# Optimization experiments

Measured on AMD Instinct MI355X. Metric: run time of the kernel, lower is better.

## Reference

```python
import jax, jax.numpy as jnp
import numpy as np

IN_DIMS = 512
TOKEN_DIM = 512
NUM_HEADS = 1
D = TOKEN_DIM * NUM_HEADS
SCALE = TOKEN_DIM ** (-0.5)
EPS = 1e-12  # torch F.normalize default


def _l2norm(v, axis):
    n = jnp.sqrt(jnp.sum(v * v, axis=axis, keepdims=True))
    return v / jnp.maximum(n, EPS)


def setup_inputs() -> dict:
    key = jax.random.key(0)
    ks = jax.random.split(key, 10)
    B, C, H, W = 64, IN_DIMS, 28, 28
    s_in = IN_DIMS ** -0.5
    s_d = D ** -0.5
    return {
        "x": jax.random.normal(ks[0], (B, C, H, W), jnp.float32),
        "Wq": jax.random.normal(ks[1], (IN_DIMS, D), jnp.float32) * s_in,
        "bq": jax.random.normal(ks[2], (D,), jnp.float32) * 0.01,
        "Wk": jax.random.normal(ks[3], (IN_DIMS, D), jnp.float32) * s_in,
        "bk": jax.random.normal(ks[4], (D,), jnp.float32) * 0.01,
        "w_g": jax.random.normal(ks[5], (D, 1), jnp.float32),
        "Wp": jax.random.normal(ks[6], (D, D), jnp.float32) * s_d,
        "bp": jax.random.normal(ks[7], (D,), jnp.float32) * 0.01,
        "Wf": jax.random.normal(ks[8], (D, TOKEN_DIM), jnp.float32) * s_d,
        "bf": jax.random.normal(ks[9], (TOKEN_DIM,), jnp.float32) * 0.01,
    }


def reference(x, Wq, bq, Wk, bk, w_g, Wp, bp, Wf, bf):
    B, C, H, W = x.shape
    t = x.reshape(B, C, H * W).transpose(0, 2, 1)          # [B, N, C]
    query = _l2norm(t @ Wq + bq, axis=-1)                  # [B, N, D]
    k = _l2norm(t @ Wk + bk, axis=-1)                      # [B, N, D]
    attn = _l2norm((query @ w_g) * SCALE, axis=1)          # [B, N, 1], normalized over tokens
    ctx = jnp.sum(attn * query, axis=1, keepdims=True)     # [B, 1, D] global context
    out = (ctx * k) @ Wp + bp + query                      # [B, N, D]
    out = out @ Wf + bf                                    # [B, N, TOKEN_DIM]
    return out.transpose(0, 2, 1).reshape(B, -1, H, W)
```

## Files before the change

kernel.cpp:

```cpp
#include <hip/hip_runtime.h>

#define EPSN 1e-12f
#define SCALE_F 0.044194173824159216f
#define MTOT 50176

typedef __bf16 bf16x8 __attribute__((ext_vector_type(8)));
typedef float  f32x4  __attribute__((ext_vector_type(4)));

__device__ __forceinline__ void gld16(const void* src, void* dst) {
  __builtin_amdgcn_global_load_lds(
      (const __attribute__((address_space(1))) unsigned int*)src,
      (__attribute__((address_space(3))) unsigned int*)dst, 16, 0, 0);
}

__global__ __launch_bounds__(256) void k_xt(const float* __restrict__ x,
                                            __bf16* __restrict__ xT, int b0) {
  __shared__ float T[32][33];
  const int n0 = blockIdx.x * 32, c0 = blockIdx.y * 32;
  const int bl = blockIdx.z, b = b0 + bl;
  const int dx = threadIdx.x, ty = threadIdx.y;
  #pragma unroll
  for (int pp = 0; pp < 4; ++pp) {
    int c = ty + pp * 8;
    int n = n0 + dx;
    T[c][dx] = (n < 784) ? x[((size_t)b * 512 + c0 + c) * 784 + n] : 0.f;
  }
  __syncthreads();
  #pragma unroll
  for (int pp = 0; pp < 4; ++pp) {
    int n = ty + pp * 8;
    if (n0 + n < 784)
      xT[((size_t)bl * 784 + n0 + n) * 512 + c0 + dx] = (__bf16)T[dx][n];
  }
}

__global__ __launch_bounds__(256) void k_prep_t(const float* __restrict__ Wq,
                                                const float* __restrict__ Wk,
                                                __bf16* __restrict__ WqT,
                                                __bf16* __restrict__ WkT) {
  __shared__ float Tq[32][33], Tk[32][33];
  const int c0 = blockIdx.x * 32, d0 = blockIdx.y * 32;
  const int dx = threadIdx.x, cy = threadIdx.y;
  #pragma unroll
  for (int p = 0; p < 4; ++p) {
    int c = cy + p * 8;
    Tq[c][dx] = Wq[(size_t)(c0 + c) * 512 + d0 + dx];
    Tk[c][dx] = Wk[(size_t)(c0 + c) * 512 + d0 + dx];
  }
  __syncthreads();
  #pragma unroll
  for (int p = 0; p < 4; ++p) {
    int d = cy + p * 8;
    WqT[(size_t)(d0 + d) * 512 + c0 + dx] = (__bf16)Tq[dx][d];
    WkT[(size_t)(d0 + d) * 512 + c0 + dx] = (__bf16)Tk[dx][d];
  }
}

__global__ __launch_bounds__(512) void k_prep_w(const float* __restrict__ Wp,
                                                const float* __restrict__ Wf,
                                                const float* __restrict__ bp,
                                                const float* __restrict__ bfv,
                                                __bf16* __restrict__ WcT,
                                                float* __restrict__ bpf) {
  const int kk0 = blockIdx.x * 8;
  const int d = threadIdx.x;
  float acc[8] = {};
  float bacc = 0.f;
  const bool dobp = (blockIdx.x == 0);
  for (int c = 0; c < 512; ++c) {
    float wf = Wf[(size_t)c * 512 + d];
    #pragma unroll
    for (int i = 0; i < 8; ++i) acc[i] = fmaf(Wp[(size_t)(kk0 + i) * 512 + c], wf, acc[i]);
    if (dobp) bacc = fmaf(bp[c], wf, bacc);
  }
  #pragma unroll
  for (int i = 0; i < 8; ++i) {
    WcT[(size_t)d * 1024 + kk0 + i]       = (__bf16)acc[i];
    WcT[(size_t)d * 1024 + 512 + kk0 + i] = (__bf16)Wf[(size_t)(kk0 + i) * 512 + d];
  }
  if (dobp) bpf[d] = bacc + bfv[d];
}

__global__ __launch_bounds__(256, 2) void k_gemm(const __bf16* __restrict__ xT,
                                                 const __bf16* __restrict__ WqT,
                                                 const __bf16* __restrict__ WkT,
                                                 const float* __restrict__ bq,
                                                 const float* __restrict__ bk,
                                                 const float* __restrict__ wg,
                                                 const int b0,
                                                 __bf16* __restrict__ qraw,
                                                 __bf16* __restrict__ kraw,
                                                 float* __restrict__ psqQ,
                                                 float* __restrict__ psqK,
                                                 float* __restrict__ gdo) {
  __shared__ __align__(1024) unsigned char As[8192], BQs[8192], BKs[8192];
  const int t = threadIdx.x, l = t & 63, w = t >> 6;
  const int li = l & 15, lq = l >> 4;
  const int p = blockIdx.x;
  const int xq = p & 7, q2 = p >> 3;
  const int nt = q2 & 3;
  const int g = (q2 >> 2) * 8 + xq;
  const int bl = g / 7, mt = g % 7;
  const int b = b0 + bl;
  const int m0 = mt * 128;

  const int r0 = 2 * w, r1 = r0 + 1;
  int row0 = m0 + r0 * 16 + li; if (row0 > 783) row0 = 783;
  int row1 = m0 + r1 * 16 + li; if (row1 > 783) row1 = 783;
  const __bf16* a0s = xT + ((size_t)bl * 784 + row0) * 512 + lq * 8;
  const __bf16* a1s = xT + ((size_t)bl * 784 + row1) * 512 + lq * 8;
  const __bf16* q0s = WqT + (size_t)(nt * 128 + r0 * 16 + li) * 512 + lq * 8;
  const __bf16* q1s = WqT + (size_t)(nt * 128 + r1 * 16 + li) * 512 + lq * 8;
  const __bf16* k0s = WkT + (size_t)(nt * 128 + r0 * 16 + li) * 512 + lq * 8;
  const __bf16* k1s = WkT + (size_t)(nt * 128 + r1 * 16 + li) * 512 + lq * 8;

  f32x4 accQ[4][4] = {}, accK[4][4] = {};

  for (int ks = 0; ks < 16; ++ks) {
    const int k0 = ks * 32;
    gld16(a0s + k0, As + r0 * 1024);
    gld16(a1s + k0, As + r1 * 1024);
    gld16(q0s + k0, BQs + r0 * 1024);
    gld16(q1s + k0, BQs + r1 * 1024);
    gld16(k0s + k0, BKs + r0 * 1024);
    gld16(k1s + k0, BKs + r1 * 1024);
    __syncthreads();
    bf16x8 af[4];
    #pragma unroll
    for (int rb = 0; rb < 4; ++rb)
      af[rb] = *(const bf16x8*)(As + ((w & 1) * 4 + rb) * 1024 + l * 16);
    #pragma unroll
    for (int cb = 0; cb < 4; ++cb) {
      bf16x8 bq8 = *(const bf16x8*)(BQs + ((w >> 1) * 4 + cb) * 1024 + l * 16);
      #pragma unroll
      for (int rb = 0; rb < 4; ++rb)
        accQ[rb][cb] = __builtin_amdgcn_mfma_f32_16x16x32_bf16(af[rb], bq8, accQ[rb][cb], 0, 0, 0);
      bf16x8 bk8 = *(const bf16x8*)(BKs + ((w >> 1) * 4 + cb) * 1024 + l * 16);
      #pragma unroll
      for (int rb = 0; rb < 4; ++rb)
        accK[rb][cb] = __builtin_amdgcn_mfma_f32_16x16x32_bf16(af[rb], bk8, accK[rb][cb], 0, 0, 0);
    }
    __syncthreads();
  }

  const int colb = nt * 128 + (w >> 1) * 64;
  const int cg = nt * 2 + (w >> 1);
  float bqv[4], bkv[4], wv[4];
  #pragma unroll
  for (int cb = 0; cb < 4; ++cb) {
    int col = colb + cb * 16 + li;
    bqv[cb] = bq[col]; bkv[cb] = bk[col]; wv[cb] = wg[col];
  }
  #pragma unroll
  for (int rb = 0; rb < 4; ++rb)
    #pragma unroll
    for (int j = 0; j < 4; ++j) {
      int rowg = m0 + (w & 1) * 64 + rb * 16 + lq * 4 + j;
      bool ok = rowg < 784;
      size_t token = (size_t)b * 784 + rowg;
      float ssq = 0.f, ssk = 0.f, sg = 0.f;
      #pragma unroll
      for (int cb = 0; cb < 4; ++cb) {
        float vq = accQ[rb][cb][j] + bqv[cb];
        float vk = accK[rb][cb][j] + bkv[cb];
        ssq = fmaf(vq, vq, ssq);
        ssk = fmaf(vk, vk, ssk);
        sg  = fmaf(vq, wv[cb], sg);
        if (ok) {
          qraw[token * 512 + colb + cb * 16 + li] = (__bf16)vq;
          kraw[token * 512 + colb + cb * 16 + li] = (__bf16)vk;
        }
      }
      ssq += __shfl_xor(ssq, 1); ssq += __shfl_xor(ssq, 2); ssq += __shfl_xor(ssq, 4); ssq += __shfl_xor(ssq, 8);
      ssk += __shfl_xor(ssk, 1); ssk += __shfl_xor(ssk, 2); ssk += __shfl_xor(ssk, 4); ssk += __shfl_xor(ssk, 8);
      sg  += __shfl_xor(sg, 1);  sg  += __shfl_xor(sg, 2);  sg  += __shfl_xor(sg, 4);  sg  += __shfl_xor(sg, 8);
      if (ok && li == 0) {
        psqQ[(size_t)cg * MTOT + token] = ssq;
        psqK[(size_t)cg * MTOT + token] = ssk;
        gdo [(size_t)cg * MTOT + token] = sg;
      }
    }
}

__global__ __launch_bounds__(256) void k_normc(const float* __restrict__ psqQ,
                                               const float* __restrict__ psqK,
                                               const float* __restrict__ gdo,
                                               float* __restrict__ invqA,
                                               float* __restrict__ invkA,
                                               float* __restrict__ coefA,
                                               float* __restrict__ gA) {
  const int tkn = blockIdx.x * 256 + threadIdx.x;
  if (tkn >= MTOT) return;
  float sq = 0.f, sk = 0.f, gd = 0.f;
  #pragma unroll
  for (int cg = 0; cg < 8; ++cg) {
    sq += psqQ[(size_t)cg * MTOT + tkn];
    sk += psqK[(size_t)cg * MTOT + tkn];
    gd += gdo[(size_t)cg * MTOT + tkn];
  }
  float invq = 1.f / fmaxf(sqrtf(sq), EPSN);
  float invk = 1.f / fmaxf(sqrtf(sk), EPSN);
  float gv = gd * invq;
  invqA[tkn] = invq;
  invkA[tkn] = invk;
  coefA[tkn] = gv * invq;
  gA[tkn]    = gv;
}

__global__ __launch_bounds__(512) void k_pctx(const __bf16* __restrict__ qraw,
                                              const float* __restrict__ coefA,
                                              const float* __restrict__ gA,
                                              float* __restrict__ ctx) {
  __shared__ float wred[8];
  __shared__ float part[4][128];
  const int ch = blockIdx.x, b = blockIdx.y, t = threadIdx.x;
  const size_t base = (size_t)b * 784;
  float gsq;
  { float gv = gA[base + t]; gsq = gv * gv; }
  if (t + 512 < 784) { float gv = gA[base + t + 512]; gsq = fmaf(gv, gv, gsq); }
  gsq += __shfl_xor(gsq, 1);  gsq += __shfl_xor(gsq, 2);  gsq += __shfl_xor(gsq, 4);
  gsq += __shfl_xor(gsq, 8);  gsq += __shfl_xor(gsq, 16); gsq += __shfl_xor(gsq, 32);
  if ((t & 63) == 0) wred[t >> 6] = gsq;
  __syncthreads();
  float tot = 0.f;
  #pragma unroll
  for (int i = 0; i < 8; ++i) tot += wred[i];
  const float alpha = SCALE_F / fmaxf(sqrtf(tot) * SCALE_F, EPSN);
  const int dof = t & 127, s = t >> 7;
  const int nb = s * 196;
  const __bf16* qb = qraw + (base + nb) * 512 + ch * 128 + dof;
  const float* cf = coefA + base + nb;
  float a0 = 0.f, a1 = 0.f, a2 = 0.f, a3 = 0.f;
  for (int n = 0; n < 196; n += 4) {
    a0 = fmaf(cf[n],     (float)qb[(size_t)n * 512],       a0);
    a1 = fmaf(cf[n + 1], (float)qb[(size_t)(n + 1) * 512], a1);
    a2 = fmaf(cf[n + 2], (float)qb[(size_t)(n + 2) * 512], a2);
    a3 = fmaf(cf[n + 3], (float)qb[(size_t)(n + 3) * 512], a3);
  }
  part[s][dof] = (a0 + a1) + (a2 + a3);
  __syncthreads();
  if (t < 128) {
    float sum = part[0][t] + part[1][t] + part[2][t] + part[3][t];
    ctx[(size_t)b * 512 + ch * 128 + t] = alpha * sum;
  }
}

__global__ __launch_bounds__(256, 3) void k_out(const __bf16* __restrict__ qraw,
                                                const __bf16* __restrict__ kraw,
                                                const float* __restrict__ invqA,
                                                const float* __restrict__ invkA,
                                                const float* __restrict__ ctx,
                                                const __bf16* __restrict__ WcT,
                                                const float* __restrict__ bpf,
                                                float* __restrict__ out) {
  __shared__ __align__(1024) unsigned char As[8192], Bs[8192];
  __shared__ float ctx_l[512];
  const int t = threadIdx.x, l = t & 63, w = t >> 6;
  const int li = l & 15, lq = l >> 4;
  const int p = blockIdx.x;
  const int xq = p & 7, q2 = p >> 3;
  const int nt = q2 & 3;
  const int g = (q2 >> 2) * 8 + xq;
  const int b = g / 7, mt = g % 7;
  const int m0 = mt * 128;

  ctx_l[t]       = ctx[(size_t)b * 512 + t];
  ctx_l[t + 256] = ctx[(size_t)b * 512 + t + 256];

  const int rA0 = w, rA1 = w + 4;
  int row0 = m0 + rA0 * 16 + li; if (row0 > 783) row0 = 783;
  int row1 = m0 + rA1 * 16 + li; if (row1 > 783) row1 = 783;
  const size_t tk0 = (size_t)b * 784 + row0, tk1 = (size_t)b * 784 + row1;
  const float iq0 = invqA[tk0], ik0 = invkA[tk0];
  const float iq1 = invqA[tk1], ik1 = invkA[tk1];
  const __bf16* wpB0 = WcT + (size_t)(nt * 128 + (2 * w) * 16 + li) * 1024 + lq * 8;
  const __bf16* wpB1 = WcT + (size_t)(nt * 128 + (2 * w + 1) * 16 + li) * 1024 + lq * 8;

  f32x4 acc[4][4] = {};
  __syncthreads();

  for (int ks = 0; ks < 32; ++ks) {
    const int k0 = ks * 32;
    gld16(wpB0 + k0, Bs + (2 * w) * 1024);
    gld16(wpB1 + k0, Bs + (2 * w + 1) * 1024);
    {
      const bool dk = ks < 16;
      const __bf16* ap = dk ? kraw : qraw;
      const int kk = (k0 & 511) + lq * 8;
      bf16x8 v0 = *(const bf16x8*)(ap + tk0 * 512 + kk);
      bf16x8 v1 = *(const bf16x8*)(ap + tk1 * 512 + kk);
      const float s0 = dk ? ik0 : iq0, s1 = dk ? ik1 : iq1;
      bf16x8 o0, o1;
      if (dk) {
        f32x4 c0 = *(const f32x4*)&ctx_l[kk];
        f32x4 c1 = *(const f32x4*)&ctx_l[kk + 4];
        #pragma unroll
        for (int j = 0; j < 4; ++j) {
          o0[j]     = (__bf16)((float)v0[j]     * s0 * c0[j]);
          o0[4 + j] = (__bf16)((float)v0[4 + j] * s0 * c1[j]);
          o1[j]     = (__bf16)((float)v1[j]     * s1 * c0[j]);
          o1[4 + j] = (__bf16)((float)v1[4 + j] * s1 * c1[j]);
        }
      } else {
        #pragma unroll
        for (int j = 0; j < 8; ++j) {
          o0[j] = (__bf16)((float)v0[j] * s0);
          o1[j] = (__bf16)((float)v1[j] * s1);
        }
      }
      *(bf16x8*)(As + rA0 * 1024 + l * 16) = o0;
      *(bf16x8*)(As + rA1 * 1024 + l * 16) = o1;
    }
    __syncthreads();
    bf16x8 af[4];
    #pragma unroll
    for (int rb = 0; rb < 4; ++rb)
      af[rb] = *(const bf16x8*)(As + ((w & 1) * 4 + rb) * 1024 + l * 16);
    #pragma unroll
    for (int cb = 0; cb < 4; ++cb) {
      bf16x8 bf = *(const bf16x8*)(Bs + ((w >> 1) * 4 + cb) * 1024 + l * 16);
      #pragma unroll
      for (int rb = 0; rb < 4; ++rb)
        acc[rb][cb] = __builtin_amdgcn_mfma_f32_16x16x32_bf16(af[rb], bf, acc[rb][cb], 0, 0, 0);
    }
    __syncthreads();
  }

  const int colb = nt * 128 + (w >> 1) * 64;
  float bv[4];
  #pragma unroll
  for (int cb = 0; cb < 4; ++cb) bv[cb] = bpf[colb + cb * 16 + li];
  #pragma unroll
  for (int rb = 0; rb < 4; ++rb) {
    int nrow = m0 + (w & 1) * 64 + rb * 16 + lq * 4;
    if (nrow < 784) {
      #pragma unroll
      for (int cb = 0; cb < 4; ++cb) {
        f32x4 v;
        #pragma unroll
        for (int j = 0; j < 4; ++j) v[j] = acc[rb][cb][j] + bv[cb];
        *(f32x4*)&out[((size_t)b * 512 + colb + cb * 16 + li) * 784 + nrow] = v;
      }
    }
  }
}

extern "C" void kernel_launch(void* const* d_in, const int* in_sizes, int n_in,
                              void* d_out, int out_size, void* d_ws, size_t ws_size,
                              hipStream_t stream) {
  const float* x   = (const float*)d_in[0];
  const float* Wq  = (const float*)d_in[1];
  const float* bq  = (const float*)d_in[2];
  const float* Wk  = (const float*)d_in[3];
  const float* bk  = (const float*)d_in[4];
  const float* wg  = (const float*)d_in[5];
  const float* Wp  = (const float*)d_in[6];
  const float* bp  = (const float*)d_in[7];
  const float* Wf  = (const float*)d_in[8];
  const float* bfv = (const float*)d_in[9];
  float* out = (float*)d_out;
  char* ws = (char*)d_ws;

  const size_t SZRAW = (size_t)MTOT * 512 * 2;
  const size_t SZXT  = (size_t)32 * 784 * 512 * 2;
  size_t off = 0;
  __bf16* qraw = (__bf16*)(ws + off); off += SZRAW;
  __bf16* kraw = (__bf16*)(ws + off); off += SZRAW;
  __bf16* xT   = (__bf16*)(ws + off); off += SZXT;
  __bf16* WqT  = (__bf16*)(ws + off); off += 524288;
  __bf16* WkT  = (__bf16*)(ws + off); off += 524288;
  __bf16* WcT  = (__bf16*)(ws + off); off += 1048576;
  float*  bpf  = (float*) (ws + off); off += 2048;
  float*  psqQ = (float*) (ws + off); off += (size_t)8 * MTOT * 4;
  float*  psqK = (float*) (ws + off); off += (size_t)8 * MTOT * 4;
  float*  gdo  = (float*) (ws + off); off += (size_t)8 * MTOT * 4;
  float*  invqA = (float*)(ws + off); off += (size_t)MTOT * 4;
  float*  invkA = (float*)(ws + off); off += (size_t)MTOT * 4;
  float*  coefA = (float*)(ws + off); off += (size_t)MTOT * 4;
  float*  gA    = (float*)(ws + off); off += (size_t)MTOT * 4;
  float*  ctx   = (float*)(ws + off); off += 131072;

  k_prep_t<<<dim3(16, 16), dim3(32, 8), 0, stream>>>(Wq, Wk, WqT, WkT);
  k_prep_w<<<dim3(64),     dim3(512),   0, stream>>>(Wp, Wf, bp, bfv, WcT, bpf);
  for (int s = 0; s < 2; ++s) {
    k_xt  <<<dim3(25, 16, 32), dim3(32, 8), 0, stream>>>(x, xT, s * 32);
    k_gemm<<<dim3(896),        dim3(256),   0, stream>>>(xT, WqT, WkT, bq, bk, wg, s * 32,
                                                         qraw, kraw, psqQ, psqK, gdo);
  }
  k_normc<<<dim3(196),   dim3(256), 0, stream>>>(psqQ, psqK, gdo, invqA, invkA, coefA, gA);
  k_pctx <<<dim3(4, 64), dim3(512), 0, stream>>>(qraw, coefA, gA, ctx);
  k_out  <<<dim3(1792),  dim3(256), 0, stream>>>(qraw, kraw, invqA, invkA, ctx, WcT, bpf, out);
}
```

Before: 408.8 us.

## Double-buffer LDS staging in GEMM kernels and widen weight prep grid

Both the q/k projection GEMM and the output GEMM now use two LDS stage buffers. The next k-slice is loaded asynchronously while MFMAs run on the current one, which leaves one barrier per iteration instead of two. In the output kernel, the global loads of the A operand (k or q rows scaled by the norms and ctx) are issued before the MFMA step and written to LDS afterwards. The weight-fusion prep kernel handles 2 rows per block instead of 8 and launches 4x more blocks to raise parallelism. The changes double LDS use per block, which may cut occupancy, and add register pressure from the prefetched values held across the MFMA step.

```diff
diff --git a/kernel.cpp b/kernel.cpp
--- a/kernel.cpp
+++ b/kernel.cpp
@@ -62,22 +62,20 @@
                                                 const float* __restrict__ bfv,
                                                 __bf16* __restrict__ WcT,
                                                 float* __restrict__ bpf) {
-  const int kk0 = blockIdx.x * 8;
+  const int kk0 = blockIdx.x * 2;
   const int d = threadIdx.x;
-  float acc[8] = {};
-  float bacc = 0.f;
+  float acc0 = 0.f, acc1 = 0.f, bacc = 0.f;
   const bool dobp = (blockIdx.x == 0);
   for (int c = 0; c < 512; ++c) {
     float wf = Wf[(size_t)c * 512 + d];
-    #pragma unroll
-    for (int i = 0; i < 8; ++i) acc[i] = fmaf(Wp[(size_t)(kk0 + i) * 512 + c], wf, acc[i]);
+    acc0 = fmaf(Wp[(size_t)kk0 * 512 + c],       wf, acc0);
+    acc1 = fmaf(Wp[(size_t)(kk0 + 1) * 512 + c], wf, acc1);
     if (dobp) bacc = fmaf(bp[c], wf, bacc);
   }
-  #pragma unroll
-  for (int i = 0; i < 8; ++i) {
-    WcT[(size_t)d * 1024 + kk0 + i]       = (__bf16)acc[i];
-    WcT[(size_t)d * 1024 + 512 + kk0 + i] = (__bf16)Wf[(size_t)(kk0 + i) * 512 + d];
-  }
+  WcT[(size_t)d * 1024 + kk0]           = (__bf16)acc0;
+  WcT[(size_t)d * 1024 + kk0 + 1]       = (__bf16)acc1;
+  WcT[(size_t)d * 1024 + 512 + kk0]     = (__bf16)Wf[(size_t)kk0 * 512 + d];
+  WcT[(size_t)d * 1024 + 512 + kk0 + 1] = (__bf16)Wf[(size_t)(kk0 + 1) * 512 + d];
   if (dobp) bpf[d] = bacc + bfv[d];
 }
 
@@ -93,7 +91,7 @@
                                                  float* __restrict__ psqQ,
                                                  float* __restrict__ psqK,
                                                  float* __restrict__ gdo) {
-  __shared__ __align__(1024) unsigned char As[8192], BQs[8192], BKs[8192];
+  __shared__ __align__(1024) unsigned char stg[2][24576];
   const int t = threadIdx.x, l = t & 63, w = t >> 6;
   const int li = l & 15, lq = l >> 4;
   const int p = blockIdx.x;
@@ -116,31 +114,45 @@
 
   f32x4 accQ[4][4] = {}, accK[4][4] = {};
 
-  for (int ks = 0; ks < 16; ++ks) {
-    const int k0 = ks * 32;
-    gld16(a0s + k0, As + r0 * 1024);
-    gld16(a1s + k0, As + r1 * 1024);
-    gld16(q0s + k0, BQs + r0 * 1024);
-    gld16(q1s + k0, BQs + r1 * 1024);
-    gld16(k0s + k0, BKs + r0 * 1024);
-    gld16(k1s + k0, BKs + r1 * 1024);
-    __syncthreads();
+  auto stage = [&](int buf, int ks) {
+    const int kk = (ks > 15 ? 15 : ks) * 32;
+    gld16(a0s + kk, stg[buf] + r0 * 1024);
+    gld16(a1s + kk, stg[buf] + r1 * 1024);
+    gld16(q0s + kk, stg[buf] + 8192 + r0 * 1024);
+    gld16(q1s + kk, stg[buf] + 8192 + r1 * 1024);
+    gld16(k0s + kk, stg[buf] + 16384 + r0 * 1024);
+    gld16(k1s + kk, stg[buf] + 16384 + r1 * 1024);
+  };
+  auto mstep = [&](int buf) {
     bf16x8 af[4];
     #pragma unroll
     for (int rb = 0; rb < 4; ++rb)
-      af[rb] = *(const bf16x8*)(As + ((w & 1) * 4 + rb) * 1024 + l * 16);
+      af[rb] = *(const bf16x8*)(stg[buf] + ((w & 1) * 4 + rb) * 1024 + l * 16);
     #pragma unroll
     for (int cb = 0; cb < 4; ++cb) {
-      bf16x8 bq8 = *(const bf16x8*)(BQs + ((w >> 1) * 4 + cb) * 1024 + l * 16);
+      bf16x8 bq8 = *(const bf16x8*)(stg[buf] + 8192 + ((w >> 1) * 4 + cb) * 1024 + l * 16);
       #pragma unroll
       for (int rb = 0; rb < 4; ++rb)
         accQ[rb][cb] = __builtin_amdgcn_mfma_f32_16x16x32_bf16(af[rb], bq8, accQ[rb][cb], 0, 0, 0);
-      bf16x8 bk8 = *(const bf16x8*)(BKs + ((w >> 1) * 4 + cb) * 1024 + l * 16);
+      bf16x8 bk8 = *(const bf16x8*)(stg[buf] + 16384 + ((w >> 1) * 4 + cb) * 1024 + l * 16);
       #pragma unroll
       for (int rb = 0; rb < 4; ++rb)
         accK[rb][cb] = __builtin_amdgcn_mfma_f32_16x16x32_bf16(af[rb], bk8, accK[rb][cb], 0, 0, 0);
     }
-    __syncthreads();
+  };
+
+  stage(0, 0);
+  asm volatile("s_waitcnt vmcnt(0)" ::: "memory");
+  __builtin_amdgcn_s_barrier();
+  __builtin_amdgcn_sched_barrier(0);
+  #pragma unroll 1
+  for (int ks = 0; ks < 16; ++ks) {
+    stage((ks + 1) & 1, ks + 1);
+    __builtin_amdgcn_sched_barrier(0);
+    mstep(ks & 1);
+    asm volatile("s_waitcnt vmcnt(0)" ::: "memory");
+    __builtin_amdgcn_s_barrier();
+    __builtin_amdgcn_sched_barrier(0);
   }
 
   const int colb = nt * 128 + (w >> 1) * 64;
@@ -253,7 +265,7 @@
                                                 const __bf16* __restrict__ WcT,
                                                 const float* __restrict__ bpf,
                                                 float* __restrict__ out) {
-  __shared__ __align__(1024) unsigned char As[8192], Bs[8192];
+  __shared__ __align__(1024) unsigned char stg[2][16384];
   __shared__ float ctx_l[512];
   const int t = threadIdx.x, l = t & 63, w = t >> 6;
   const int li = l & 15, lq = l >> 4;
@@ -266,6 +278,7 @@
 
   ctx_l[t]       = ctx[(size_t)b * 512 + t];
   ctx_l[t + 256] = ctx[(size_t)b * 512 + t + 256];
+  __syncthreads();
 
   const int rA0 = w, rA1 = w + 4;
   int row0 = m0 + rA0 * 16 + li; if (row0 > 783) row0 = 783;
@@ -277,53 +290,79 @@
   const __bf16* wpB1 = WcT + (size_t)(nt * 128 + (2 * w + 1) * 16 + li) * 1024 + lq * 8;
 
   f32x4 acc[4][4] = {};
-  __syncthreads();
-
-  for (int ks = 0; ks < 32; ++ks) {
-    const int k0 = ks * 32;
-    gld16(wpB0 + k0, Bs + (2 * w) * 1024);
-    gld16(wpB1 + k0, Bs + (2 * w + 1) * 1024);
-    {
-      const bool dk = ks < 16;
-      const __bf16* ap = dk ? kraw : qraw;
-      const int kk = (k0 & 511) + lq * 8;
-      bf16x8 v0 = *(const bf16x8*)(ap + tk0 * 512 + kk);
-      bf16x8 v1 = *(const bf16x8*)(ap + tk1 * 512 + kk);
-      const float s0 = dk ? ik0 : iq0, s1 = dk ? ik1 : iq1;
-      bf16x8 o0, o1;
-      if (dk) {
-        f32x4 c0 = *(const f32x4*)&ctx_l[kk];
-        f32x4 c1 = *(const f32x4*)&ctx_l[kk + 4];
-        #pragma unroll
-        for (int j = 0; j < 4; ++j) {
-          o0[j]     = (__bf16)((float)v0[j]     * s0 * c0[j]);
-          o0[4 + j] = (__bf16)((float)v0[4 + j] * s0 * c1[j]);
-          o1[j]     = (__bf16)((float)v1[j]     * s1 * c0[j]);
-          o1[4 + j] = (__bf16)((float)v1[4 + j] * s1 * c1[j]);
-        }
-      } else {
-        #pragma unroll
-        for (int j = 0; j < 8; ++j) {
-          o0[j] = (__bf16)((float)v0[j] * s0);
-          o1[j] = (__bf16)((float)v1[j] * s1);
-        }
+
+  auto stageB = [&](int buf, int ks) {
+    const int kk = (ks > 31 ? 31 : ks) * 32;
+    gld16(wpB0 + kk, stg[buf] + 8192 + (2 * w) * 1024);
+    gld16(wpB1 + kk, stg[buf] + 8192 + (2 * w + 1) * 1024);
+  };
+  auto loadA = [&](bf16x8& v0, bf16x8& v1, int ks) {
+    const int kk = ks > 31 ? 31 : ks;
+    const __bf16* ap = (kk < 16) ? kraw : qraw;
+    const int off = (kk & 15) * 32 + lq * 8;
+    v0 = *(const bf16x8*)(ap + tk0 * 512 + off);
+    v1 = *(const bf16x8*)(ap + tk1 * 512 + off);
+  };
+  auto writeA = [&](int buf, bf16x8 v0, bf16x8 v1, int ks) {
+    const int kk = ks > 31 ? 31 : ks;
+    bf16x8 o0, o1;
+    if (kk < 16) {
+      const int kl = (kk & 15) * 32 + lq * 8;
+      f32x4 c0 = *(const f32x4*)&ctx_l[kl];
+      f32x4 c1 = *(const f32x4*)&ctx_l[kl + 4];
+      #pragma unroll
+      for (int j = 0; j < 4; ++j) {
+        o0[j]     = (__bf16)((float)v0[j]     * ik0 * c0[j]);
+        o0[4 + j] = (__bf16)((float)v0[4 + j] * ik0 * c1[j]);
+        o1[j]     = (__bf16)((float)v1[j]     * ik1 * c0[j]);
+        o1[4 + j] = (__bf16)((float)v1[4 + j] * ik1 * c1[j]);
       }
-      *(bf16x8*)(As + rA0 * 1024 + l * 16) = o0;
-      *(bf16x8*)(As + rA1 * 1024 + l * 16) = o1;
+    } else {
+      #pragma unroll
+      for (int j = 0; j < 8; ++j) {
+        o0[j] = (__bf16)((float)v0[j] * iq0);
+        o1[j] = (__bf16)((float)v1[j] * iq1);
+      }
     }
-    __syncthreads();
+    *(bf16x8*)(stg[buf] + rA0 * 1024 + l * 16) = o0;
+    *(bf16x8*)(stg[buf] + rA1 * 1024 + l * 16) = o1;
+  };
+  auto mstep = [&](int buf) {
     bf16x8 af[4];
     #pragma unroll
     for (int rb = 0; rb < 4; ++rb)
-      af[rb] = *(const bf16x8*)(As + ((w & 1) * 4 + rb) * 1024 + l * 16);
+      af[rb] = *(const bf16x8*)(stg[buf] + ((w & 1) * 4 + rb) * 1024 + l * 16);
     #pragma unroll
     for (int cb = 0; cb < 4; ++cb) {
-      bf16x8 bf = *(const bf16x8*)(Bs + ((w >> 1) * 4 + cb) * 1024 + l * 16);
+      bf16x8 bf = *(const bf16x8*)(stg[buf] + 8192 + ((w >> 1) * 4 + cb) * 1024 + l * 16);
       #pragma unroll
       for (int rb = 0; rb < 4; ++rb)
         acc[rb][cb] = __builtin_amdgcn_mfma_f32_16x16x32_bf16(af[rb], bf, acc[rb][cb], 0, 0, 0);
     }
-    __syncthreads();
+  };
+
+  {
+    bf16x8 vA0, vA1;
+    loadA(vA0, vA1, 0);
+    stageB(0, 0);
+    asm volatile("s_waitcnt vmcnt(0)" ::: "memory");
+    writeA(0, vA0, vA1, 0);
+    asm volatile("s_waitcnt lgkmcnt(0)" ::: "memory");
+    __builtin_amdgcn_s_barrier();
+    __builtin_amdgcn_sched_barrier(0);
+  }
+  #pragma unroll 1
+  for (int ks = 0; ks < 32; ++ks) {
+    bf16x8 nA0, nA1;
+    loadA(nA0, nA1, ks + 1);
+    stageB((ks + 1) & 1, ks + 1);
+    __builtin_amdgcn_sched_barrier(0);
+    mstep(ks & 1);
+    asm volatile("s_waitcnt vmcnt(0)" ::: "memory");
+    writeA((ks + 1) & 1, nA0, nA1, ks + 1);
+    asm volatile("s_waitcnt lgkmcnt(0)" ::: "memory");
+    __builtin_amdgcn_s_barrier();
+    __builtin_amdgcn_sched_barrier(0);
   }
 
   const int colb = nt * 128 + (w >> 1) * 64;
@@ -381,7 +420,7 @@
   float*  ctx   = (float*)(ws + off); off += 131072;
 
   k_prep_t<<<dim3(16, 16), dim3(32, 8), 0, stream>>>(Wq, Wk, WqT, WkT);
-  k_prep_w<<<dim3(64),     dim3(512),   0, stream>>>(Wp, Wf, bp, bfv, WcT, bpf);
+  k_prep_w<<<dim3(256),    dim3(512),   0, stream>>>(Wp, Wf, bp, bfv, WcT, bpf);
   for (int s = 0; s < 2; ++s) {
     k_xt  <<<dim3(25, 16, 32), dim3(32, 8), 0, stream>>>(x, xT, s * 32);
     k_gemm<<<dim3(896),        dim3(256),   0, stream>>>(xT, WqT, WkT, bq, bk, wg, s * 32,
```

Result: no change. 402.4 us (-1.6%).
